# Kernel optimization log

Hardware: AMD Instinct MI355X
Metric: run time of the kernel (lower is better)

## Reference

```python
import jax, jax.numpy as jnp
import numpy as np

B, S, D, H = 2, 2048, 1280, 16
DEPTH = D // H  # 80


def setup_inputs() -> dict:
    key = jax.random.key(0)
    ks = jax.random.split(key, 6)
    scale = 1.0 / np.sqrt(D)
    x = jax.random.normal(ks[0], (B, S, D), dtype=jnp.float32)
    # causal mask: 1.0 where attention is disallowed (strict upper triangle)
    mask = jnp.triu(jnp.ones((S, S), dtype=jnp.float32), k=1)
    Wq = jax.random.normal(ks[1], (D, D), dtype=jnp.float32) * scale
    Wk = jax.random.normal(ks[2], (D, D), dtype=jnp.float32) * scale
    Wv = jax.random.normal(ks[3], (D, D), dtype=jnp.float32) * scale
    Wo = jax.random.normal(ks[4], (D, D), dtype=jnp.float32) * scale
    z = jnp.zeros((D,), dtype=jnp.float32)
    return {"x": x, "mask": mask, "Wq": Wq, "bq": z, "Wk": Wk, "bk": z,
            "Wv": Wv, "bv": z, "Wo": Wo, "bo": z}


def _split_heads(t):
    # [B, S, D] -> [B, H, S, depth]
    return t.reshape(B, -1, H, DEPTH).transpose(0, 2, 1, 3)


def reference(x, mask, Wq, bq, Wk, bk, Wv, bv, Wo, bo):
    q = _split_heads(x @ Wq + bq)
    k = _split_heads(x @ Wk + bk)
    v = _split_heads(x @ Wv + bv)
    # scaled dot-product attention with additive (masked * -10000) logits
    logits = jnp.einsum("bhqd,bhkd->bhqk", q, k) / jnp.sqrt(
        jnp.asarray(DEPTH, dtype=jnp.float32))
    logits = logits + mask * -10000.0  # mask broadcasts over [B, H]
    attn = jax.nn.softmax(logits, axis=-1)
    ctx = jnp.einsum("bhqk,bhkd->bhqd", attn, v)
    ctx = ctx.transpose(0, 2, 1, 3).reshape(B, -1, D)  # merge heads
    return ctx @ Wo + bo
```

## Files before the change

### kernel.cpp

```cpp
#include <hip/hip_runtime.h>

typedef unsigned short u16;
typedef __bf16 bf16;
typedef __bf16 bf16x8 __attribute__((ext_vector_type(8)));
typedef unsigned short u16x8 __attribute__((ext_vector_type(8)));
typedef unsigned short u16x4 __attribute__((ext_vector_type(4)));
typedef float f32x4 __attribute__((ext_vector_type(4)));

constexpr int B_ = 2, S_ = 2048, D_ = 1280, H_ = 16, DEPTH_ = 80;
constexpr int M_ = B_ * S_;
constexpr int QR_ = 128;

__device__ inline u16 f2b(float f) { return __builtin_bit_cast(u16, (bf16)f); }

typedef __attribute__((address_space(1))) const void gvoid;
typedef __attribute__((address_space(3))) void lvoid;
__device__ inline void gl_lds16(const void* g, void* l) {
  __builtin_amdgcn_global_load_lds((gvoid*)g, (lvoid*)l, 16, 0, 0);
}

__global__ __launch_bounds__(256) void prep_k(const float* __restrict__ x,
                                              u16* __restrict__ xbf,
                                              u16* __restrict__ QK,
                                              const float* __restrict__ W0,
                                              const float* __restrict__ W1,
                                              const float* __restrict__ W2,
                                              const float* __restrict__ W3,
                                              u16* __restrict__ WT) {
  __shared__ u16 t[32][33];
  int bid = blockIdx.x, tid = threadIdx.x;
  if (bid < 2560) {
    int i0 = (bid * 256 + tid) * 8;
    u16x8 v;
#pragma unroll
    for (int j = 0; j < 8; ++j) v[j] = f2b(x[i0 + j]);
    *(u16x8*)(xbf + i0) = v;
  } else if (bid < 5632) {
    int c = (bid - 2560) * 256 + tid;
    int r = c / 6, k = c - r * 6;
    u16x8 z = {};
    *(u16x8*)(QK + (size_t)r * QR_ + 80 + k * 8) = z;
  } else {
    int tt = bid - 5632;
    int z = tt / 1600, w = tt - z * 1600;
    int x0 = (w % 40) * 32, y0 = (w / 40) * 32;
    const float* srcs[4] = {W0, W1, W2, W3};
    const float* W = srcs[z];
    u16* out = WT + (size_t)z * D_ * D_;
    int tx = tid & 31, ty = tid >> 5;
#pragma unroll
    for (int i = 0; i < 4; ++i)
      t[ty + 8 * i][tx] = f2b(W[(size_t)(y0 + ty + 8 * i) * D_ + x0 + tx]);
    __syncthreads();
#pragma unroll
    for (int i = 0; i < 4; ++i)
      out[(size_t)(x0 + ty + 8 * i) * D_ + y0 + tx] = t[tx][ty + 8 * i];
  }
}

struct GemmAcc {
  f32x4 acc[4][4];
};
__device__ inline void gemm_core(const u16* __restrict__ A,
                                 const u16* __restrict__ BT, int m0, int n0,
                                 u16* a_s, u16* b_s, GemmAcc& g) {
  int tid = threadIdx.x, lane = tid & 63, wave = tid >> 6;
  int quad = lane >> 4, l15 = lane & 15;
  int wm = wave >> 1, wn = wave & 1;
  int r4 = lane >> 2, c4 = (lane & 3) * 8;

  for (int k0 = 0; k0 < D_; k0 += 32) {
    __syncthreads();
#pragma unroll
    for (int j = 0; j < 2; ++j) {
      int ch = wave * 2 + j;
      gl_lds16(A + (size_t)(m0 + ch * 16 + r4) * D_ + k0 + c4, a_s + ch * 512);
      gl_lds16(BT + (size_t)(n0 + ch * 16 + r4) * D_ + k0 + c4, b_s + ch * 512);
    }
    __syncthreads();
    bf16x8 af[4], bfr[4];
#pragma unroll
    for (int mt = 0; mt < 4; ++mt)
      af[mt] = *(const bf16x8*)(a_s + (wm * 64 + mt * 16 + l15) * 32 + quad * 8);
#pragma unroll
    for (int nt = 0; nt < 4; ++nt)
      bfr[nt] = *(const bf16x8*)(b_s + (wn * 64 + nt * 16 + l15) * 32 + quad * 8);
#pragma unroll
    for (int mt = 0; mt < 4; ++mt)
#pragma unroll
      for (int nt = 0; nt < 4; ++nt)
        g.acc[mt][nt] = __builtin_amdgcn_mfma_f32_16x16x32_bf16(
            af[mt], bfr[nt], g.acc[mt][nt], 0, 0, 0);
  }
}

__global__ __launch_bounds__(256, 4) void gemm_out(const u16* __restrict__ A,
                                                   const u16* __restrict__ BT,
                                                   const float* __restrict__ bias,
                                                   float* __restrict__ out) {
  __shared__ __align__(16) u16 a_s[128 * 32];
  __shared__ __align__(16) u16 b_s[128 * 32];
  int lane = threadIdx.x & 63, wave = threadIdx.x >> 6;
  int quad = lane >> 4, l15 = lane & 15;
  int wm = wave >> 1, wn = wave & 1;
  int m0 = blockIdx.y * 128, n0 = blockIdx.x * 128;

  GemmAcc g = {};
  gemm_core(A, BT, m0, n0, a_s, b_s, g);

#pragma unroll
  for (int nt = 0; nt < 4; ++nt) {
    int col = n0 + wn * 64 + nt * 16 + l15;
    float bv = bias[col];
#pragma unroll
    for (int mt = 0; mt < 4; ++mt)
#pragma unroll
      for (int r = 0; r < 4; ++r) {
        int row = m0 + wm * 64 + mt * 16 + quad * 4 + r;
        out[(size_t)row * D_ + col] = g.acc[mt][nt][r] + bv;
      }
  }
}

__device__ inline void stage_half(const u16* __restrict__ gsrc, int half,
                                  u16* lbase, int wave, int lane) {
  int rl = lane >> 3, c8 = lane & 7;
  int sc = (c8 ^ rl) << 3;
#pragma unroll
  for (int i = 0; i < 2; ++i) {
    int j = half * 16 + wave * 2 + i;
    gl_lds16(gsrc + (size_t)(j * 8 + rl) * D_ + sc, lbase + j * 512);
  }
}

__device__ inline bf16x8 frd(const u16* b, int r, int g) {
  return *(const bf16x8*)(b + r * 64 + ((g ^ (r & 7)) << 3));
}

__global__ __launch_bounds__(512, 2) void gemm_qkv8(
    const u16* __restrict__ A, const u16* __restrict__ BT,
    const float* __restrict__ bq, const float* __restrict__ bk,
    const float* __restrict__ bv, u16* __restrict__ Qw, u16* __restrict__ Kw,
    u16* __restrict__ Vw) {
  __shared__ __align__(16) u16 AS[2][256 * 64];
  __shared__ __align__(16) u16 BS[2][256 * 64];
  constexpr int BK = 64, NT = D_ / BK;
  int tid = threadIdx.x, lane = tid & 63, wave = tid >> 6;
  int quad = lane >> 4, l15 = lane & 15;
  int wm = wave >> 2, wn = wave & 3;
  int bid = blockIdx.x;
  int sw = (bid & 7) * 30 + (bid >> 3);
  int by = sw / 15, bx = sw - by * 15;
  int m0 = by * 256, n0 = bx * 256;
  const u16* Ab = A + (size_t)m0 * D_;
  const u16* Bb = BT + (size_t)n0 * D_;

  f32x4 acc[8][4] = {};

  stage_half(Ab, 0, (u16*)AS[0], wave, lane);
  stage_half(Ab, 1, (u16*)AS[0], wave, lane);
  stage_half(Bb, 0, (u16*)BS[0], wave, lane);
  stage_half(Bb, 1, (u16*)BS[0], wave, lane);
  stage_half(Bb + BK, 0, (u16*)BS[1], wave, lane);
  stage_half(Bb + BK, 1, (u16*)BS[1], wave, lane);
  asm volatile("s_waitcnt vmcnt(4)" ::: "memory");
  __builtin_amdgcn_s_barrier();

  bf16x8 a[4][2], bl[2][2], bh[2][2];
  int ra = wm * 128 + l15, rb = wn * 64 + l15;

#pragma unroll 2
  for (int T = 0; T < NT; ++T) {
    const u16* Ac = AS[T & 1];
    const u16* Bc = BS[T & 1];
    u16* An = (u16*)AS[(T + 1) & 1];
    u16* Bcur = (u16*)BS[T & 1];

#pragma unroll
    for (int mt = 0; mt < 4; ++mt)
#pragma unroll
      for (int kh = 0; kh < 2; ++kh)
        a[mt][kh] = frd(Ac, ra + mt * 16, kh * 4 + quad);
#pragma unroll
    for (int nt = 0; nt < 2; ++nt)
#pragma unroll
      for (int kh = 0; kh < 2; ++kh)
        bl[nt][kh] = frd(Bc, rb + nt * 16, kh * 4 + quad);
    if (T + 1 < NT) stage_half(Ab + (size_t)(T + 1) * BK, 0, An, wave, lane);
    asm volatile("" ::: "memory");
    __builtin_amdgcn_s_barrier();
    __builtin_amdgcn_s_setprio(1);
#pragma unroll
    for (int mt = 0; mt < 4; ++mt)
#pragma unroll
      for (int nt = 0; nt < 2; ++nt)
#pragma unroll
        for (int kh = 0; kh < 2; ++kh)
          acc[mt][nt] = __builtin_amdgcn_mfma_f32_16x16x32_bf16(
              a[mt][kh], bl[nt][kh], acc[mt][nt], 0, 0, 0);
    __builtin_amdgcn_s_setprio(0);
    asm volatile("" ::: "memory");
    __builtin_amdgcn_s_barrier();

#pragma unroll
    for (int nt = 0; nt < 2; ++nt)
#pragma unroll
      for (int kh = 0; kh < 2; ++kh)
        bh[nt][kh] = frd(Bc, rb + 32 + nt * 16, kh * 4 + quad);
    if (T + 1 < NT) stage_half(Ab + (size_t)(T + 1) * BK, 1, An, wave, lane);
    asm volatile("" ::: "memory");
    __builtin_amdgcn_s_barrier();
    __builtin_amdgcn_s_setprio(1);
#pragma unroll
    for (int mt = 0; mt < 4; ++mt)
#pragma unroll
      for (int nt = 0; nt < 2; ++nt)
#pragma unroll
        for (int kh = 0; kh < 2; ++kh)
          acc[mt][nt + 2] = __builtin_amdgcn_mfma_f32_16x16x32_bf16(
              a[mt][kh], bh[nt][kh], acc[mt][nt + 2], 0, 0, 0);
    __builtin_amdgcn_s_setprio(0);
    asm volatile("" ::: "memory");
    __builtin_amdgcn_s_barrier();

#pragma unroll
    for (int mt = 0; mt < 4; ++mt)
#pragma unroll
      for (int kh = 0; kh < 2; ++kh)
        a[mt][kh] = frd(Ac, ra + 64 + mt * 16, kh * 4 + quad);
    if (T + 2 < NT) stage_half(Bb + (size_t)(T + 2) * BK, 0, Bcur, wave, lane);
    asm volatile("" ::: "memory");
    __builtin_amdgcn_s_barrier();
    __builtin_amdgcn_s_setprio(1);
#pragma unroll
    for (int mt = 0; mt < 4; ++mt)
#pragma unroll
      for (int nt = 0; nt < 2; ++nt)
#pragma unroll
        for (int kh = 0; kh < 2; ++kh)
          acc[mt + 4][nt + 2] = __builtin_amdgcn_mfma_f32_16x16x32_bf16(
              a[mt][kh], bh[nt][kh], acc[mt + 4][nt + 2], 0, 0, 0);
    __builtin_amdgcn_s_setprio(0);
    asm volatile("" ::: "memory");
    __builtin_amdgcn_s_barrier();

    if (T + 2 < NT) stage_half(Bb + (size_t)(T + 2) * BK, 1, Bcur, wave, lane);
    asm volatile("" ::: "memory");
    __builtin_amdgcn_s_barrier();
    __builtin_amdgcn_s_setprio(1);
#pragma unroll
    for (int mt = 0; mt < 4; ++mt)
#pragma unroll
      for (int nt = 0; nt < 2; ++nt)
#pragma unroll
        for (int kh = 0; kh < 2; ++kh)
          acc[mt + 4][nt] = __builtin_amdgcn_mfma_f32_16x16x32_bf16(
              a[mt][kh], bl[nt][kh], acc[mt + 4][nt], 0, 0, 0);
    __builtin_amdgcn_s_setprio(0);
    if (T < NT - 2)
      asm volatile("s_waitcnt vmcnt(4)" ::: "memory");
    else if (T == NT - 2)
      asm volatile("s_waitcnt vmcnt(0)" ::: "memory");
    asm volatile("" ::: "memory");
    __builtin_amdgcn_s_barrier();
  }

  int mat = n0 / D_;
  if (mat == 2) {
#pragma unroll
    for (int nt = 0; nt < 4; ++nt) {
      int co = n0 + wn * 64 + nt * 16 + l15 - 2 * D_;
      float bb_ = bv[co];
      int h = co / DEPTH_, d = co % DEPTH_;
#pragma unroll
      for (int mt = 0; mt < 8; ++mt) {
        int row = m0 + wm * 128 + mt * 16 + quad * 4;
        int b = row >> 11, s = row & (S_ - 1);
        u16x4 pk;
#pragma unroll
        for (int r = 0; r < 4; ++r) pk[r] = f2b(acc[mt][nt][r] + bb_);
        *(u16x4*)(Vw + ((size_t)(b * H_ + h) * DEPTH_ + d) * S_ + s) = pk;
      }
    }
  } else {
    const float* bp = (mat == 0) ? bq : bk;
    u16* outp = mat ? Kw : Qw;
#pragma unroll
    for (int nt = 0; nt < 4; ++nt) {
      int co = n0 + wn * 64 + nt * 16 + l15 - mat * D_;
      float bb_ = bp[co];
      int h = co / DEPTH_, d = co % DEPTH_;
#pragma unroll
      for (int mt = 0; mt < 8; ++mt)
#pragma unroll
        for (int r = 0; r < 4; ++r) {
          int row = m0 + wm * 128 + mt * 16 + quad * 4 + r;
          int b = row >> 11, s = row & (S_ - 1);
          outp[((size_t)(b * H_ + h) * S_ + s) * QR_ + d] =
              f2b(acc[mt][nt][r] + bb_);
        }
    }
  }
}

__device__ inline void attn_stage(const u16* __restrict__ Kb,
                                  const u16* __restrict__ Vb, int k0, u16* ks,
                                  u16* vs, int wave, int lane) {
  int quad = lane >> 4, l15 = lane & 15;
#pragma unroll
  for (int i = 0; i < 2; ++i) {
    int row = (wave * 2 + i) * 4 + quad;
    int sc = l15 ^ (row & 7);
    gl_lds16(Kb + (size_t)(k0 + row) * QR_ + sc * 8,
             ks + (size_t)row * QR_ + l15 * 8);
  }
#pragma unroll
  for (int i = 0; i < 2; ++i) {
    int j = wave + 8 * i;
    if (j < 10) {
      int ch = j * 64 + lane;
      int row = ch >> 3, pos = ch & 7;
      int sc = pos ^ (row & 7);
      gl_lds16(Vb + (size_t)row * S_ + k0 + sc * 8, vs + ch * 8);
    }
  }
}

__global__ __launch_bounds__(512, 2) void attn_k(const u16* __restrict__ Qp,
                                                 const u16* __restrict__ Kp,
                                                 const u16* __restrict__ VT,
                                                 u16* __restrict__ ctx) {
  constexpr float SCALE = 0.11180339887498949f;
  __shared__ __align__(16) u16 k_s[2][64 * 128];
  __shared__ __align__(16) u16 vt_s[2][80 * 64];
  __shared__ __align__(16) u16 p_s[128 * 72];
  int tid = threadIdx.x, lane = tid & 63, wave = tid >> 6;
  int quad = lane >> 4, l15 = lane & 15;
  int bid = blockIdx.x;
  int bh = bid & 31, bx = bid >> 5;
  const u16* Qb = Qp + (size_t)bh * S_ * QR_;
  const u16* Kb = Kp + (size_t)bh * S_ * QR_;
  const u16* Vb = VT + (size_t)bh * DEPTH_ * S_;
  int b = bh >> 4, h = bh & 15;

#pragma unroll 1
  for (int t = 0; t < 2; ++t) {
    int qt = t ? (15 - bx) : bx;
    int nkt = 2 * qt + 2;

    bf16x8 qf[3];
#pragma unroll
    for (int ks = 0; ks < 3; ++ks)
      qf[ks] = *(const bf16x8*)(Qb + (size_t)(qt * 128 + wave * 16 + l15) * QR_ +
                                ks * 32 + quad * 8);
    f32x4 acc_o[5] = {};
    float lsum[4] = {};

    attn_stage(Kb, Vb, 0, k_s[0], vt_s[0], wave, lane);
    asm volatile("s_waitcnt vmcnt(0)" ::: "memory");
    __syncthreads();

    for (int kt = 0; kt < nkt; ++kt) {
      int k0 = kt * 64;
      int cur = kt & 1;
      if (kt + 1 < nkt)
        attn_stage(Kb, Vb, k0 + 64, k_s[cur ^ 1], vt_s[cur ^ 1], wave, lane);
      const u16* ksb = k_s[cur];
      const u16* vsb = vt_s[cur];

      f32x4 sa[4] = {};
#pragma unroll
      for (int ks = 0; ks < 3; ++ks) {
        int pa = ((ks * 4 + quad) ^ (l15 & 7)) * 8;
#pragma unroll
        for (int nt = 0; nt < 4; ++nt) {
          bf16x8 bfr = *(const bf16x8*)(ksb + (size_t)(nt * 16 + l15) * QR_ + pa);
          sa[nt] =
              __builtin_amdgcn_mfma_f32_16x16x32_bf16(qf[ks], bfr, sa[nt], 0, 0, 0);
        }
      }
      bool diag = (kt >= 2 * qt);
#pragma unroll
      for (int nt = 0; nt < 4; ++nt)
#pragma unroll
        for (int r = 0; r < 4; ++r) {
          float p = __expf(sa[nt][r] * SCALE);
          if (diag &&
              (k0 + nt * 16 + l15) > (qt * 128 + wave * 16 + quad * 4 + r))
            p = 0.0f;
          sa[nt][r] = p;
          lsum[r] += p;
        }
      asm volatile("s_waitcnt lgkmcnt(0)" ::: "memory");
#pragma unroll
      for (int nt = 0; nt < 4; ++nt)
#pragma unroll
        for (int r = 0; r < 4; ++r)
          p_s[(wave * 16 + quad * 4 + r) * 72 + nt * 16 + l15] = f2b(sa[nt][r]);
      asm volatile("s_waitcnt lgkmcnt(0)" ::: "memory");
#pragma unroll
      for (int kk = 0; kk < 2; ++kk) {
        bf16x8 af =
            *(const bf16x8*)(p_s + (wave * 16 + l15) * 72 + kk * 32 + quad * 8);
#pragma unroll
        for (int d5 = 0; d5 < 5; ++d5) {
          int pv = ((kk * 4 + quad) ^ (l15 & 7)) * 8;
          bf16x8 bfr = *(const bf16x8*)(vsb + (size_t)(d5 * 16 + l15) * 64 + pv);
          acc_o[d5] =
              __builtin_amdgcn_mfma_f32_16x16x32_bf16(af, bfr, acc_o[d5], 0, 0, 0);
        }
      }
      asm volatile("s_waitcnt vmcnt(0)" ::: "memory");
      __syncthreads();
    }

    float ls[4];
#pragma unroll
    for (int r = 0; r < 4; ++r) {
      ls[r] = lsum[r];
#pragma unroll
      for (int m = 1; m < 16; m <<= 1) ls[r] += __shfl_xor(ls[r], m, 16);
    }
#pragma unroll
    for (int d5 = 0; d5 < 5; ++d5)
#pragma unroll
      for (int r = 0; r < 4; ++r) {
        int s = qt * 128 + wave * 16 + quad * 4 + r;
        int col = h * DEPTH_ + d5 * 16 + l15;
        ctx[(size_t)(b * S_ + s) * D_ + col] = f2b(acc_o[d5][r] / ls[r]);
      }
  }
}

extern "C" void kernel_launch(void* const* d_in, const int* in_sizes, int n_in,
                              void* d_out, int out_size, void* d_ws, size_t ws_size,
                              hipStream_t stream) {
  const float* x  = (const float*)d_in[0];
  const float* Wq = (const float*)d_in[2];
  const float* bq = (const float*)d_in[3];
  const float* Wk = (const float*)d_in[4];
  const float* bk = (const float*)d_in[5];
  const float* Wv = (const float*)d_in[6];
  const float* bv = (const float*)d_in[7];
  const float* Wo = (const float*)d_in[8];
  const float* bo = (const float*)d_in[9];

  const size_t DD = (size_t)D_ * D_;
  const size_t QE = (size_t)B_ * H_ * S_ * DEPTH_;
  const size_t QP = (size_t)B_ * H_ * S_ * QR_;
  u16* xbf = (u16*)d_ws;
  u16* wT  = xbf + QE;
  u16* Qw  = wT + 4 * DD;
  u16* Kw  = Qw + QP;
  u16* Vw  = Kw + QP;
  u16* Cw  = xbf;
  size_t need = (size_t)(Vw + QE - xbf) * 2;
  if (ws_size < need) return;

  prep_k<<<12032, 256, 0, stream>>>(x, xbf, Qw, Wq, Wk, Wv, Wo, wT);
  gemm_qkv8<<<240, 512, 0, stream>>>(xbf, wT, bq, bk, bv, Qw, Kw, Vw);
  attn_k<<<256, 512, 0, stream>>>(Qw, Kw, Vw, Cw);
  gemm_out<<<dim3(D_ / 128, M_ / 128), 256, 0, stream>>>(Cw, wT + 3 * DD, bo,
                                                         (float*)d_out);
}
```

Baseline: 257.0 us.

## Split attention KV tiles across two wave classes, each wave covering 32 query rows

Reorganizes the attention kernel so each wave handles 32 query rows (two 16-row MFMA tiles) and the two groups of four waves alternately process even and odd KV tiles, then combines their partial outputs and row sums through shared memory at the end. K/V fragments loaded from LDS are reused across two query tiles, halving LDS reads per MFMA, and the P buffer uses an XOR-swizzled layout. The exponential now uses exp2 with a prescaled constant. In exchange, register pressure rises (launch-bounds occupancy hint dropped), half the waves idle on each tile step, and an extra LDS reduction and barriers are added.

```diff
diff --git a/kernel.cpp b/kernel.cpp
--- a/kernel.cpp
+++ b/kernel.cpp
@@ -326,16 +326,19 @@
   }
 }
 
-__global__ __launch_bounds__(512, 2) void attn_k(const u16* __restrict__ Qp,
-                                                 const u16* __restrict__ Kp,
-                                                 const u16* __restrict__ VT,
-                                                 u16* __restrict__ ctx) {
-  constexpr float SCALE = 0.11180339887498949f;
-  __shared__ __align__(16) u16 k_s[2][64 * 128];
-  __shared__ __align__(16) u16 vt_s[2][80 * 64];
-  __shared__ __align__(16) u16 p_s[128 * 72];
+__global__ __launch_bounds__(512) void attn_k(const u16* __restrict__ Qp,
+                                              const u16* __restrict__ Kp,
+                                              const u16* __restrict__ VT,
+                                              u16* __restrict__ ctx) {
+  constexpr float SC2 = 0.16129820f;
+  __shared__ __align__(16) u16 sh[43008];
+  u16* k_s0 = sh;
+  u16* vt_s0 = sh + 16384;
+  u16* p_s = sh + 26624;
+  float* cmb = (float*)sh;
   int tid = threadIdx.x, lane = tid & 63, wave = tid >> 6;
   int quad = lane >> 4, l15 = lane & 15;
+  int g = wave & 3, cls = wave >> 2;
   int bid = blockIdx.x;
   int bh = bid & 31, bx = bid >> 5;
   const u16* Qb = Qp + (size_t)bh * S_ * QR_;
@@ -348,15 +351,18 @@
     int qt = t ? (15 - bx) : bx;
     int nkt = 2 * qt + 2;
 
-    bf16x8 qf[3];
-#pragma unroll
-    for (int ks = 0; ks < 3; ++ks)
-      qf[ks] = *(const bf16x8*)(Qb + (size_t)(qt * 128 + wave * 16 + l15) * QR_ +
-                                ks * 32 + quad * 8);
-    f32x4 acc_o[5] = {};
-    float lsum[4] = {};
-
-    attn_stage(Kb, Vb, 0, k_s[0], vt_s[0], wave, lane);
+    bf16x8 qf[2][3];
+#pragma unroll
+    for (int m = 0; m < 2; ++m)
+#pragma unroll
+      for (int ks = 0; ks < 3; ++ks)
+        qf[m][ks] = *(const bf16x8*)(
+            Qb + (size_t)(qt * 128 + g * 32 + m * 16 + l15) * QR_ + ks * 32 +
+            quad * 8);
+    f32x4 acc_o[2][5] = {};
+    float lsum[2][4] = {};
+
+    attn_stage(Kb, Vb, 0, k_s0, vt_s0, wave, lane);
     asm volatile("s_waitcnt vmcnt(0)" ::: "memory");
     __syncthreads();
 
@@ -364,71 +370,117 @@
       int k0 = kt * 64;
       int cur = kt & 1;
       if (kt + 1 < nkt)
-        attn_stage(Kb, Vb, k0 + 64, k_s[cur ^ 1], vt_s[cur ^ 1], wave, lane);
-      const u16* ksb = k_s[cur];
-      const u16* vsb = vt_s[cur];
-
-      f32x4 sa[4] = {};
-#pragma unroll
-      for (int ks = 0; ks < 3; ++ks) {
-        int pa = ((ks * 4 + quad) ^ (l15 & 7)) * 8;
-#pragma unroll
-        for (int nt = 0; nt < 4; ++nt) {
-          bf16x8 bfr = *(const bf16x8*)(ksb + (size_t)(nt * 16 + l15) * QR_ + pa);
-          sa[nt] =
-              __builtin_amdgcn_mfma_f32_16x16x32_bf16(qf[ks], bfr, sa[nt], 0, 0, 0);
+        attn_stage(Kb, Vb, k0 + 64, k_s0 + (cur ^ 1) * 8192,
+                   vt_s0 + (cur ^ 1) * 5120, wave, lane);
+      if (cls == cur) {
+        const u16* ksb = k_s0 + cur * 8192;
+        const u16* vsb = vt_s0 + cur * 5120;
+        f32x4 sa[2][4] = {};
+#pragma unroll
+        for (int ks = 0; ks < 3; ++ks) {
+          int pa = ((ks * 4 + quad) ^ (l15 & 7)) * 8;
+#pragma unroll
+          for (int nt = 0; nt < 4; ++nt) {
+            bf16x8 bfr = *(const bf16x8*)(ksb + (size_t)(nt * 16 + l15) * QR_ + pa);
+            sa[0][nt] = __builtin_amdgcn_mfma_f32_16x16x32_bf16(qf[0][ks], bfr,
+                                                                sa[0][nt], 0, 0, 0);
+            sa[1][nt] = __builtin_amdgcn_mfma_f32_16x16x32_bf16(qf[1][ks], bfr,
+                                                                sa[1][nt], 0, 0, 0);
+          }
         }
-      }
-      bool diag = (kt >= 2 * qt);
-#pragma unroll
-      for (int nt = 0; nt < 4; ++nt)
-#pragma unroll
-        for (int r = 0; r < 4; ++r) {
-          float p = __expf(sa[nt][r] * SCALE);
-          if (diag &&
-              (k0 + nt * 16 + l15) > (qt * 128 + wave * 16 + quad * 4 + r))
-            p = 0.0f;
-          sa[nt][r] = p;
-          lsum[r] += p;
-        }
-      asm volatile("s_waitcnt lgkmcnt(0)" ::: "memory");
-#pragma unroll
-      for (int nt = 0; nt < 4; ++nt)
-#pragma unroll
-        for (int r = 0; r < 4; ++r)
-          p_s[(wave * 16 + quad * 4 + r) * 72 + nt * 16 + l15] = f2b(sa[nt][r]);
-      asm volatile("s_waitcnt lgkmcnt(0)" ::: "memory");
-#pragma unroll
-      for (int kk = 0; kk < 2; ++kk) {
-        bf16x8 af =
-            *(const bf16x8*)(p_s + (wave * 16 + l15) * 72 + kk * 32 + quad * 8);
-#pragma unroll
-        for (int d5 = 0; d5 < 5; ++d5) {
+        bool diag = (kt >= 2 * qt);
+#pragma unroll
+        for (int m = 0; m < 2; ++m)
+#pragma unroll
+          for (int nt = 0; nt < 4; ++nt)
+#pragma unroll
+            for (int r = 0; r < 4; ++r) {
+              float p = __builtin_amdgcn_exp2f(sa[m][nt][r] * SC2);
+              if (diag && (k0 + nt * 16 + l15) >
+                              (qt * 128 + g * 32 + m * 16 + quad * 4 + r))
+                p = 0.0f;
+              sa[m][nt][r] = p;
+              lsum[m][r] += p;
+            }
+        asm volatile("s_waitcnt lgkmcnt(0)" ::: "memory");
+#pragma unroll
+        for (int m = 0; m < 2; ++m)
+#pragma unroll
+          for (int nt = 0; nt < 4; ++nt)
+#pragma unroll
+            for (int r = 0; r < 4; ++r) {
+              int row = g * 32 + m * 16 + quad * 4 + r;
+              int cgp = (nt * 2 + (l15 >> 3)) ^ (row & 15);
+              p_s[row * 128 + cgp * 8 + (l15 & 7)] = f2b(sa[m][nt][r]);
+            }
+        asm volatile("s_waitcnt lgkmcnt(0)" ::: "memory");
+#pragma unroll
+        for (int kk = 0; kk < 2; ++kk) {
+          bf16x8 af[2];
+#pragma unroll
+          for (int m = 0; m < 2; ++m) {
+            int rr = g * 32 + m * 16 + l15;
+            int cgp = (kk * 4 + quad) ^ (rr & 15);
+            af[m] = *(const bf16x8*)(p_s + rr * 128 + cgp * 8);
+          }
           int pv = ((kk * 4 + quad) ^ (l15 & 7)) * 8;
-          bf16x8 bfr = *(const bf16x8*)(vsb + (size_t)(d5 * 16 + l15) * 64 + pv);
-          acc_o[d5] =
-              __builtin_amdgcn_mfma_f32_16x16x32_bf16(af, bfr, acc_o[d5], 0, 0, 0);
+#pragma unroll
+          for (int d5 = 0; d5 < 5; ++d5) {
+            bf16x8 vfr = *(const bf16x8*)(vsb + (size_t)(d5 * 16 + l15) * 64 + pv);
+            acc_o[0][d5] = __builtin_amdgcn_mfma_f32_16x16x32_bf16(
+                af[0], vfr, acc_o[0][d5], 0, 0, 0);
+            acc_o[1][d5] = __builtin_amdgcn_mfma_f32_16x16x32_bf16(
+                af[1], vfr, acc_o[1][d5], 0, 0, 0);
+          }
         }
       }
       asm volatile("s_waitcnt vmcnt(0)" ::: "memory");
       __syncthreads();
     }
 
-    float ls[4];
-#pragma unroll
-    for (int r = 0; r < 4; ++r) {
-      ls[r] = lsum[r];
-#pragma unroll
-      for (int m = 1; m < 16; m <<= 1) ls[r] += __shfl_xor(ls[r], m, 16);
-    }
-#pragma unroll
-    for (int d5 = 0; d5 < 5; ++d5)
-#pragma unroll
-      for (int r = 0; r < 4; ++r) {
-        int s = qt * 128 + wave * 16 + quad * 4 + r;
-        int col = h * DEPTH_ + d5 * 16 + l15;
-        ctx[(size_t)(b * S_ + s) * D_ + col] = f2b(acc_o[d5][r] / ls[r]);
+    int ci = (g * 64 + lane) * 49;
+    if (cls == 1) {
+#pragma unroll
+      for (int m = 0; m < 2; ++m) {
+#pragma unroll
+        for (int d5 = 0; d5 < 5; ++d5)
+#pragma unroll
+          for (int r = 0; r < 4; ++r)
+            cmb[ci + (m * 5 + d5) * 4 + r] = acc_o[m][d5][r];
+#pragma unroll
+        for (int r = 0; r < 4; ++r) cmb[ci + 40 + m * 4 + r] = lsum[m][r];
       }
+    }
+    __syncthreads();
+    if (cls == 0) {
+#pragma unroll
+      for (int m = 0; m < 2; ++m) {
+#pragma unroll
+        for (int d5 = 0; d5 < 5; ++d5)
+#pragma unroll
+          for (int r = 0; r < 4; ++r)
+            acc_o[m][d5][r] += cmb[ci + (m * 5 + d5) * 4 + r];
+#pragma unroll
+        for (int r = 0; r < 4; ++r) lsum[m][r] += cmb[ci + 40 + m * 4 + r];
+#pragma unroll
+        for (int r = 0; r < 4; ++r)
+#pragma unroll
+          for (int s = 1; s < 16; s <<= 1)
+            lsum[m][r] += __shfl_xor(lsum[m][r], s, 16);
+      }
+#pragma unroll
+      for (int m = 0; m < 2; ++m)
+#pragma unroll
+        for (int d5 = 0; d5 < 5; ++d5)
+#pragma unroll
+          for (int r = 0; r < 4; ++r) {
+            int s = qt * 128 + g * 32 + m * 16 + quad * 4 + r;
+            int col = h * DEPTH_ + d5 * 16 + l15;
+            ctx[(size_t)(b * S_ + s) * D_ + col] =
+                f2b(acc_o[m][d5][r] / lsum[m][r]);
+          }
+    }
+    __syncthreads();
   }
 }
 
```

Measured after the change: 258.6 us. About the same (+0.6%).
